# Kernel tuning notes

Hardware: AMD Instinct MI355X
Metric: run time of the kernel (lower is better)

The kernel has to match this reference:

```python
import jax, jax.numpy as jnp
import numpy as np

D_K = 64
ATTN_MASKED = True
NEG = 1.0e9


def setup_inputs() -> dict:
    key = jax.random.key(0)
    k1, k2, k3, k4 = jax.random.split(key, 4)
    B, H, S, d = 2, 16, 2048, D_K
    Q = jax.random.normal(k1, (B, H, S, d), dtype=jnp.float32)
    K = jax.random.normal(k2, (B, H, S, d), dtype=jnp.float32)
    V = jax.random.normal(k3, (B, H, S, d), dtype=jnp.float32)
    pad_mask = jax.random.randint(k4, (B, S), 0, 2, dtype=jnp.int32)
    return {"Q": Q, "K": K, "V": V, "pad_mask": pad_mask}


def reference(Q, K, V, pad_mask):
    # scores: [B, H, Sq, Sk]
    scores = jnp.einsum("bhqd,bhkd->bhqk", Q, K) / np.sqrt(D_K).astype(np.float32)
    S_out, S_in = scores.shape[-2], scores.shape[-1]
    pad = pad_mask[:, None, None, :].astype(scores.dtype)  # [B,1,1,Sk]
    if ATTN_MASKED:
        causal = jnp.triu(jnp.ones((S_out, S_in), dtype=scores.dtype), k=1)[None, None]
        mask = ((pad + causal) > 0).astype(scores.dtype)
    else:
        mask = jnp.broadcast_to(pad, scores.shape)
    scores = scores - NEG * mask
    attn = jax.nn.softmax(scores, axis=-1)
    return jnp.einsum("bhqk,bhkd->bhqd", attn, V)
```

## Files before the change

### kernel.cpp

```cpp
#include <hip/hip_runtime.h>
#include <hip/hip_bf16.h>

#define S_LEN 2048
#define DH    64
#define NBH   32
#define KVT   32
#define NT    64

typedef __attribute__((ext_vector_type(8)))  short short8;
typedef __attribute__((ext_vector_type(4)))  float f32x4;
typedef __attribute__((ext_vector_type(16))) float f32x16;

static __device__ __forceinline__ unsigned cvtpk_bf16(float a, float b) {
    unsigned r;
    asm("v_cvt_pk_bf16_f32 %0, %1, %2" : "=v"(r) : "v"(a), "v"(b));
    return r;
}
static __device__ __forceinline__ float xor32_max(float x) {
    return fmaxf(x, __shfl_xor(x, 32));
}
static __device__ __forceinline__ float xor32_add(float x) {
    return x + __shfl_xor(x, 32);
}

__global__ __launch_bounds__(256)
void prep_kernel(const float* __restrict__ K, const float* __restrict__ V,
                 char* __restrict__ Kimg, char* __restrict__ Vimg)
{
    const int t = blockIdx.x, bh = blockIdx.y, tid = threadIdx.x;
    const long tileOff = ((long)bh * NT + t) * 4096;
    const float* kp = K + (long)bh * S_LEN * DH + t * KVT * DH;
    const float* vp = V + (long)bh * S_LEN * DH + t * KVT * DH;

    {
        int key = tid >> 3, dc = tid & 7;
        f32x4 x = *(const f32x4*)(kp + key * 64 + dc * 8);
        f32x4 y = *(const f32x4*)(kp + key * 64 + dc * 8 + 4);
        uint4 w;
        w.x = cvtpk_bf16(x[0], x[1]);
        w.y = cvtpk_bf16(x[2], x[3]);
        w.z = cvtpk_bf16(y[0], y[1]);
        w.w = cvtpk_bf16(y[2], y[3]);
        *(uint4*)(Kimg + tileOff + key * 128 + dc * 16) = w;
    }
    {
        int vdg = tid & 15, vkq = tid >> 4;
        int d0 = vdg * 4, k0 = vkq * 2;
        f32x4 x0 = *(const f32x4*)(vp + k0 * 64 + d0);
        f32x4 x1 = *(const f32x4*)(vp + (k0 + 1) * 64 + d0);
        #pragma unroll
        for (int i = 0; i < 4; ++i)
            *(unsigned*)(Vimg + tileOff + (d0 + i) * 64 + k0 * 2) = cvtpk_bf16(x0[i], x1[i]);
    }
}

__global__ void fz_kernel(const int* __restrict__ pad, int* __restrict__ fz)
{
    int b = blockIdx.x;
    __shared__ int red[256];
    int local = S_LEN;
    for (int k = threadIdx.x; k < S_LEN; k += 256)
        if (pad[b * S_LEN + k] == 0 && k < local) local = k;
    red[threadIdx.x] = local;
    __syncthreads();
    for (int s = 128; s > 0; s >>= 1) {
        if (threadIdx.x < s) red[threadIdx.x] = min(red[threadIdx.x], red[threadIdx.x + s]);
        __syncthreads();
    }
    if (threadIdx.x == 0) fz[b] = red[0];
}

__global__ __launch_bounds__(1024)
void bias_kernel(const int* __restrict__ pad, float* __restrict__ bias)
{
    int b = blockIdx.x;
    #pragma unroll
    for (int i = 0; i < 2; ++i) {
        int k = threadIdx.x + i * 1024;
        bias[b * S_LEN + k] = pad[b * S_LEN + k] ? -1e30f : 0.f;
    }
}

__global__ __launch_bounds__(1024)
void meanv_kernel(const float* __restrict__ V, const int* __restrict__ fz,
                  float* __restrict__ meanv)
{
    const int bh = blockIdx.x;
    const int b  = bh >> 4;
    if (fz[b] <= 0) return;
    const int d4 = threadIdx.x & 15;
    const int kp = threadIdx.x >> 4;
    const float* vp = V + (long)bh * S_LEN * DH;
    f32x4 acc = (f32x4){0.f, 0.f, 0.f, 0.f};
    #pragma unroll 4
    for (int k = kp; k < S_LEN; k += 64)
        acc += *(const f32x4*)(vp + (long)k * DH + d4 * 4);
    __shared__ f32x4 red[64][16];
    red[kp][d4] = acc;
    __syncthreads();
    #pragma unroll
    for (int s = 32; s >= 1; s >>= 1) {
        if (kp < s) red[kp][d4] += red[kp + s][d4];
        __syncthreads();
    }
    if (kp == 0)
        *(f32x4*)(meanv + bh * DH + d4 * 4) = red[0][d4] * (1.0f / 2048.0f);
}

#define LOADK(dst, tt) do { const char* _p = KB + (long)(tt) * 4096 + lq * 128 + hi * 16; \
    dst[0] = *(const short8*)(_p);       dst[1] = *(const short8*)(_p + 32);  \
    dst[2] = *(const short8*)(_p + 64);  dst[3] = *(const short8*)(_p + 96); } while (0)
#define LOADV(dst, tt) do { const char* _p = VB + (long)(tt) * 4096 + lq * 64 + hi * 16; \
    dst[0] = *(const short8*)(_p);        dst[1] = *(const short8*)(_p + 32); \
    dst[2] = *(const short8*)(_p + 2048); dst[3] = *(const short8*)(_p + 2048 + 32); } while (0)
#define LOADB(dst, tt) do { const float* _p = biasB + (tt) * 32 + hi * 4; \
    dst[0] = *(const f32x4*)(_p);      dst[1] = *(const f32x4*)(_p + 8); \
    dst[2] = *(const f32x4*)(_p + 16); dst[3] = *(const f32x4*)(_p + 24); } while (0)

#define COMPUTE(TT, K_, V_, B_) do {                                          \
    f32x16 s0;                                                                \
    _Pragma("unroll")                                                         \
    for (int g = 0; g < 4; ++g) {                                             \
        f32x4 pb4 = B_[g];                                                    \
        _Pragma("unroll")                                                     \
        for (int i = 0; i < 4; ++i) s0[g * 4 + i] = pb4[i];                   \
    }                                                                         \
    __builtin_amdgcn_s_setprio(1);                                            \
    s0 = __builtin_amdgcn_mfma_f32_32x32x16_bf16(K_[0], bq[0], s0, 0, 0, 0);  \
    s0 = __builtin_amdgcn_mfma_f32_32x32x16_bf16(K_[1], bq[1], s0, 0, 0, 0);  \
    s0 = __builtin_amdgcn_mfma_f32_32x32x16_bf16(K_[2], bq[2], s0, 0, 0, 0);  \
    s0 = __builtin_amdgcn_mfma_f32_32x32x16_bf16(K_[3], bq[3], s0, 0, 0, 0);  \
    __builtin_amdgcn_s_setprio(0);                                            \
    if ((TT) == nkv - 1) {                                                    \
        _Pragma("unroll")                                                     \
        for (int rr = 0; rr < 16; ++rr) {                                     \
            int key_r = (rr & 3) + 8 * (rr >> 2) + 4 * hi;                    \
            if (key_r > lq) s0[rr] = -1e30f;                                  \
        }                                                                     \
    }                                                                         \
    float bm = s0[0];                                                         \
    _Pragma("unroll")                                                         \
    for (int rr = 1; rr < 16; ++rr) bm = fmaxf(bm, s0[rr]);                   \
    bm = xor32_max(bm);                                                       \
    if (__any(bm > m_run + 8.0f)) {                                           \
        float mnew = fmaxf(m_run, bm);                                        \
        float c = exp2f(m_run - mnew);                                        \
        m_run = mnew; l_run *= c;                                             \
        _Pragma("unroll")                                                     \
        for (int rr = 0; rr < 16; ++rr) { o0[rr] *= c; o1[rr] *= c; }         \
    }                                                                         \
    float rs = 0.f;                                                           \
    _Pragma("unroll")                                                         \
    for (int rr = 0; rr < 16; ++rr) {                                         \
        float p = exp2f(s0[rr] - m_run);                                      \
        s0[rr] = p; rs += p;                                                  \
    }                                                                         \
    l_run += xor32_add(rs);                                                   \
    short8 pfr0, pfr1;                                                        \
    {                                                                         \
        unsigned a0 = cvtpk_bf16(s0[0], s0[1]), b0 = cvtpk_bf16(s0[4], s0[5]);\
        asm("v_permlane32_swap_b32 %0, %1" : "+v"(a0), "+v"(b0));             \
        unsigned a1 = cvtpk_bf16(s0[2], s0[3]), b1 = cvtpk_bf16(s0[6], s0[7]);\
        asm("v_permlane32_swap_b32 %0, %1" : "+v"(a1), "+v"(b1));             \
        union { short8 s8; unsigned u[4]; } u;                                \
        u.u[0] = a0; u.u[1] = a1; u.u[2] = b0; u.u[3] = b1;                   \
        pfr0 = u.s8;                                                          \
    }                                                                         \
    {                                                                         \
        unsigned a0 = cvtpk_bf16(s0[8], s0[9]),  b0 = cvtpk_bf16(s0[12], s0[13]); \
        asm("v_permlane32_swap_b32 %0, %1" : "+v"(a0), "+v"(b0));             \
        unsigned a1 = cvtpk_bf16(s0[10], s0[11]), b1 = cvtpk_bf16(s0[14], s0[15]); \
        asm("v_permlane32_swap_b32 %0, %1" : "+v"(a1), "+v"(b1));             \
        union { short8 s8; unsigned u[4]; } u;                                \
        u.u[0] = a0; u.u[1] = a1; u.u[2] = b0; u.u[3] = b1;                   \
        pfr1 = u.s8;                                                          \
    }                                                                         \
    __builtin_amdgcn_s_setprio(1);                                            \
    o0 = __builtin_amdgcn_mfma_f32_32x32x16_bf16(V_[0], pfr0, o0, 0, 0, 0);   \
    o0 = __builtin_amdgcn_mfma_f32_32x32x16_bf16(V_[1], pfr1, o0, 0, 0, 0);   \
    o1 = __builtin_amdgcn_mfma_f32_32x32x16_bf16(V_[2], pfr0, o1, 0, 0, 0);   \
    o1 = __builtin_amdgcn_mfma_f32_32x32x16_bf16(V_[3], pfr1, o1, 0, 0, 0);   \
    __builtin_amdgcn_s_setprio(0);                                            \
} while (0)

__global__ __launch_bounds__(64, 2)
void attn_fwd7(const float* __restrict__ Q, const char* __restrict__ Kimg,
               const char* __restrict__ Vimg, const float* __restrict__ bias,
               float* __restrict__ out)
{
    const int lane = threadIdx.x;
    const int lq = lane & 31, hi = lane >> 5;

    const int gid = blockIdx.x;
    const int x   = gid & 7;
    const int c   = (gid >> 3) & 31;
    const int m   = (gid >> 8) & 3;
    const int s   = gid >> 10;
    const int bh  = x + 8 * (c & 3);
    const int e   = ((c >> 2) << 2) | m;
    const int bx  = s ? 63 - e : e;
    const int q0  = bx * 32;
    const int nkv = bx + 1;
    const long base = (long)bh * S_LEN * DH;

    const char*  KB    = Kimg + (long)bh * NT * 4096;
    const char*  VB    = Vimg + (long)bh * NT * 4096;
    const float* biasB = bias + (bh >> 4) * S_LEN;

    const float QS = 0.18033688011112042f;
    short8 bq[4];
    {
        const float* qp = Q + base + (long)(q0 + lq) * DH;
        #pragma unroll
        for (int ss = 0; ss < 4; ++ss) {
            int d0 = ss * 16 + hi * 8;
            f32x4 xx = *(const f32x4*)(qp + d0);
            f32x4 yy = *(const f32x4*)(qp + d0 + 4);
            union { short8 s8; unsigned u4[4]; } uu;
            uu.u4[0] = cvtpk_bf16(xx[0] * QS, xx[1] * QS);
            uu.u4[1] = cvtpk_bf16(xx[2] * QS, xx[3] * QS);
            uu.u4[2] = cvtpk_bf16(yy[0] * QS, yy[1] * QS);
            uu.u4[3] = cvtpk_bf16(yy[2] * QS, yy[3] * QS);
            bq[ss] = uu.s8;
        }
    }

    f32x16 o0, o1;
    #pragma unroll
    for (int rr = 0; rr < 16; ++rr) { o0[rr] = 0.f; o1[rr] = 0.f; }
    float m_run = -1e30f, l_run = 0.f;

    short8 kA[4], kB_[4], kC[4], vA[4], vB_[4], vC[4];
    f32x4  bA[4], bB_[4], bC[4];

    LOADB(bA, 0);  LOADK(kA, 0);  LOADV(vA, 0);
    if (nkv > 1) { LOADB(bB_, 1); LOADK(kB_, 1); LOADV(vB_, 1); }

    int t = 0;
    for (;;) {
        if (t + 2 < nkv) { LOADB(bC, t + 2);  LOADK(kC, t + 2);  LOADV(vC, t + 2); }
        COMPUTE(t, kA, vA, bA);
        ++t; if (t >= nkv) break;
        if (t + 2 < nkv) { LOADB(bA, t + 2);  LOADK(kA, t + 2);  LOADV(vA, t + 2); }
        COMPUTE(t, kB_, vB_, bB_);
        ++t; if (t >= nkv) break;
        if (t + 2 < nkv) { LOADB(bB_, t + 2); LOADK(kB_, t + 2); LOADV(vB_, t + 2); }
        COMPUTE(t, kC, vC, bC);
        ++t; if (t >= nkv) break;
    }

    float invl = 1.0f / l_run;
    float* op = out + base + (long)(q0 + lq) * DH;
    #pragma unroll
    for (int g = 0; g < 4; ++g) {
        f32x4 w0, w1;
        #pragma unroll
        for (int i = 0; i < 4; ++i) {
            w0[i] = o0[g * 4 + i] * invl;
            w1[i] = o1[g * 4 + i] * invl;
        }
        *(f32x4*)(op + g * 8 + hi * 4)      = w0;
        *(f32x4*)(op + 32 + g * 8 + hi * 4) = w1;
    }
}

__global__ void fixup_kernel(const int* __restrict__ fz, const float* __restrict__ meanv,
                             float* __restrict__ out)
{
    const int bh = blockIdx.x;
    const int b  = bh >> 4;
    const int n  = fz[b];
    if (n <= 0) return;
    __shared__ float mv[DH];
    if (threadIdx.x < DH) mv[threadIdx.x] = meanv[bh * DH + threadIdx.x];
    __syncthreads();
    float* op = out + (long)bh * S_LEN * DH;
    for (int i = threadIdx.x; i < n * DH; i += 256) op[i] = mv[i & 63];
}

extern "C" void kernel_launch(void* const* d_in, const int* in_sizes, int n_in,
                              void* d_out, int out_size, void* d_ws, size_t ws_size,
                              hipStream_t stream)
{
    const float* Q   = (const float*)d_in[0];
    const float* K   = (const float*)d_in[1];
    const float* V   = (const float*)d_in[2];
    const int*   pad = (const int*)d_in[3];
    float* out = (float*)d_out;

    int*   fz    = (int*)d_ws;
    float* meanv = (float*)((char*)d_ws + 256);
    float* bias  = (float*)((char*)d_ws + 8448);
    char*  Kimg  = (char*)d_ws + 32768;
    char*  Vimg  = Kimg + (size_t)NBH * NT * 4096;

    fz_kernel<<<dim3(2), dim3(256), 0, stream>>>(pad, fz);
    bias_kernel<<<dim3(2), dim3(1024), 0, stream>>>(pad, bias);
    prep_kernel<<<dim3(NT, NBH), dim3(256), 0, stream>>>(K, V, Kimg, Vimg);
    attn_fwd7<<<dim3(2048), dim3(64), 0, stream>>>(Q, Kimg, Vimg, bias, out);
    meanv_kernel<<<dim3(NBH), dim3(1024), 0, stream>>>(V, fz, meanv);
    fixup_kernel<<<dim3(NBH), dim3(256), 0, stream>>>(fz, meanv, out);
}
```

Before: 94.11 us.

## Split KV loop across four waves per block with LDS softmax merge

Each block now runs four waves that stride over the KV tiles of one 32-query tile. Their partial max, sum and output accumulators are combined through shared memory by wave 0 using a flash-decoding style rescale. This targets the long serial KV loops of late causal tiles, which limited latency and parallelism with one wave per block. It adds LDS traffic, a block barrier and idle waves on short tiles. The row max and row sum reductions are also rewritten as trees to shorten the dependency chains.

```diff
diff --git a/kernel.cpp b/kernel.cpp
--- a/kernel.cpp
+++ b/kernel.cpp
@@ -138,9 +138,11 @@
             if (key_r > lq) s0[rr] = -1e30f;                                  \
         }                                                                     \
     }                                                                         \
-    float bm = s0[0];                                                         \
+    float bmg[4];                                                             \
     _Pragma("unroll")                                                         \
-    for (int rr = 1; rr < 16; ++rr) bm = fmaxf(bm, s0[rr]);                   \
+    for (int g = 0; g < 4; ++g)                                               \
+        bmg[g] = fmaxf(fmaxf(s0[g*4], s0[g*4+1]), fmaxf(s0[g*4+2], s0[g*4+3])); \
+    float bm = fmaxf(fmaxf(bmg[0], bmg[1]), fmaxf(bmg[2], bmg[3]));           \
     bm = xor32_max(bm);                                                       \
     if (__any(bm > m_run + 8.0f)) {                                           \
         float mnew = fmaxf(m_run, bm);                                        \
@@ -149,12 +151,13 @@
         _Pragma("unroll")                                                     \
         for (int rr = 0; rr < 16; ++rr) { o0[rr] *= c; o1[rr] *= c; }         \
     }                                                                         \
-    float rs = 0.f;                                                           \
     _Pragma("unroll")                                                         \
-    for (int rr = 0; rr < 16; ++rr) {                                         \
-        float p = exp2f(s0[rr] - m_run);                                      \
-        s0[rr] = p; rs += p;                                                  \
-    }                                                                         \
+    for (int rr = 0; rr < 16; ++rr) s0[rr] = exp2f(s0[rr] - m_run);           \
+    float rsg[4];                                                             \
+    _Pragma("unroll")                                                         \
+    for (int g = 0; g < 4; ++g)                                               \
+        rsg[g] = (s0[g*4] + s0[g*4+1]) + (s0[g*4+2] + s0[g*4+3]);             \
+    float rs = (rsg[0] + rsg[1]) + (rsg[2] + rsg[3]);                         \
     l_run += xor32_add(rs);                                                   \
     short8 pfr0, pfr1;                                                        \
     {                                                                         \
@@ -183,13 +186,19 @@
     __builtin_amdgcn_s_setprio(0);                                            \
 } while (0)
 
-__global__ __launch_bounds__(64, 2)
-void attn_fwd7(const float* __restrict__ Q, const char* __restrict__ Kimg,
+__global__ __launch_bounds__(256, 3)
+void attn_fwd8(const float* __restrict__ Q, const char* __restrict__ Kimg,
                const char* __restrict__ Vimg, const float* __restrict__ bias,
                float* __restrict__ out)
 {
-    const int lane = threadIdx.x;
-    const int lq = lane & 31, hi = lane >> 5;
+    __shared__ float mW[4][32];
+    __shared__ float lW[4][32];
+    __shared__ __align__(16) char ldsO[3][8192];
+
+    const int tid  = threadIdx.x;
+    const int lane = tid & 63;
+    const int w    = tid >> 6;
+    const int lq   = lane & 31, hi = lane >> 5;
 
     const int gid = blockIdx.x;
     const int x   = gid & 7;
@@ -230,37 +239,72 @@
     for (int rr = 0; rr < 16; ++rr) { o0[rr] = 0.f; o1[rr] = 0.f; }
     float m_run = -1e30f, l_run = 0.f;
 
-    short8 kA[4], kB_[4], kC[4], vA[4], vB_[4], vC[4];
-    f32x4  bA[4], bB_[4], bC[4];
-
-    LOADB(bA, 0);  LOADK(kA, 0);  LOADV(vA, 0);
-    if (nkv > 1) { LOADB(bB_, 1); LOADK(kB_, 1); LOADV(vB_, 1); }
-
-    int t = 0;
-    for (;;) {
-        if (t + 2 < nkv) { LOADB(bC, t + 2);  LOADK(kC, t + 2);  LOADV(vC, t + 2); }
-        COMPUTE(t, kA, vA, bA);
-        ++t; if (t >= nkv) break;
-        if (t + 2 < nkv) { LOADB(bA, t + 2);  LOADK(kA, t + 2);  LOADV(vA, t + 2); }
-        COMPUTE(t, kB_, vB_, bB_);
-        ++t; if (t >= nkv) break;
-        if (t + 2 < nkv) { LOADB(bB_, t + 2); LOADK(kB_, t + 2); LOADV(vB_, t + 2); }
-        COMPUTE(t, kC, vC, bC);
-        ++t; if (t >= nkv) break;
-    }
-
-    float invl = 1.0f / l_run;
-    float* op = out + base + (long)(q0 + lq) * DH;
-    #pragma unroll
-    for (int g = 0; g < 4; ++g) {
-        f32x4 w0, w1;
+    const int nw = (w < nkv) ? ((nkv - w + 3) >> 2) : 0;
+#define TIDX(i) (w + 4 * (i))
+
+    if (nw > 0) {
+        short8 kA[4], kB_[4], kC[4], vA[4], vB_[4], vC[4];
+        f32x4  bA[4], bB_[4], bC[4];
+
+        LOADB(bA, TIDX(0));  LOADK(kA, TIDX(0));  LOADV(vA, TIDX(0));
+        if (nw > 1) { LOADB(bB_, TIDX(1)); LOADK(kB_, TIDX(1)); LOADV(vB_, TIDX(1)); }
+
+        int i = 0;
+        for (;;) {
+            if (i + 2 < nw) { LOADB(bC, TIDX(i+2));  LOADK(kC, TIDX(i+2));  LOADV(vC, TIDX(i+2)); }
+            COMPUTE(TIDX(i), kA, vA, bA);
+            ++i; if (i >= nw) break;
+            if (i + 2 < nw) { LOADB(bA, TIDX(i+2));  LOADK(kA, TIDX(i+2));  LOADV(vA, TIDX(i+2)); }
+            COMPUTE(TIDX(i), kB_, vB_, bB_);
+            ++i; if (i >= nw) break;
+            if (i + 2 < nw) { LOADB(bB_, TIDX(i+2)); LOADK(kB_, TIDX(i+2)); LOADV(vB_, TIDX(i+2)); }
+            COMPUTE(TIDX(i), kC, vC, bC);
+            ++i; if (i >= nw) break;
+        }
+    }
+
+    mW[w][lq] = m_run;
+    lW[w][lq] = l_run;
+    if (w > 0) {
+        char* dst = ldsO[w - 1] + lane * 128;
         #pragma unroll
-        for (int i = 0; i < 4; ++i) {
-            w0[i] = o0[g * 4 + i] * invl;
-            w1[i] = o1[g * 4 + i] * invl;
+        for (int g = 0; g < 4; ++g) {
+            f32x4 a0, a1;
+            #pragma unroll
+            for (int i = 0; i < 4; ++i) { a0[i] = o0[g * 4 + i]; a1[i] = o1[g * 4 + i]; }
+            *(f32x4*)(dst + ((g       ^ (lane & 7)) * 16)) = a0;
+            *(f32x4*)(dst + (((4 + g) ^ (lane & 7)) * 16)) = a1;
         }
-        *(f32x4*)(op + g * 8 + hi * 4)      = w0;
-        *(f32x4*)(op + 32 + g * 8 + hi * 4) = w1;
+    }
+    __syncthreads();
+    if (w == 0) {
+        float m0 = mW[0][lq], m1 = mW[1][lq], m2 = mW[2][lq], m3 = mW[3][lq];
+        float ms = fmaxf(fmaxf(m0, m1), fmaxf(m2, m3));
+        float w0 = exp2f(m0 - ms), w1 = exp2f(m1 - ms);
+        float w2 = exp2f(m2 - ms), w3 = exp2f(m3 - ms);
+        float ls = ((w0 * lW[0][lq] + w1 * lW[1][lq]) + (w2 * lW[2][lq] + w3 * lW[3][lq]));
+        float invl = 1.0f / ls;
+
+        const char* s1p = ldsO[0] + lane * 128;
+        const char* s2p = ldsO[1] + lane * 128;
+        const char* s3p = ldsO[2] + lane * 128;
+        float* op = out + base + (long)(q0 + lq) * DH;
+        #pragma unroll
+        for (int g = 0; g < 4; ++g) {
+            int c0 = (g       ^ (lane & 7)) * 16;
+            int c1 = ((4 + g) ^ (lane & 7)) * 16;
+            f32x4 r10 = *(const f32x4*)(s1p + c0), r11 = *(const f32x4*)(s1p + c1);
+            f32x4 r20 = *(const f32x4*)(s2p + c0), r21 = *(const f32x4*)(s2p + c1);
+            f32x4 r30 = *(const f32x4*)(s3p + c0), r31 = *(const f32x4*)(s3p + c1);
+            f32x4 a0, a1;
+            #pragma unroll
+            for (int i = 0; i < 4; ++i) {
+                a0[i] = ((o0[g*4+i] * w0 + r10[i] * w1) + (r20[i] * w2 + r30[i] * w3)) * invl;
+                a1[i] = ((o1[g*4+i] * w0 + r11[i] * w1) + (r21[i] * w2 + r31[i] * w3)) * invl;
+            }
+            *(f32x4*)(op + g * 8 + hi * 4)      = a0;
+            *(f32x4*)(op + 32 + g * 8 + hi * 4) = a1;
+        }
     }
 }
 
@@ -297,7 +341,7 @@
     fz_kernel<<<dim3(2), dim3(256), 0, stream>>>(pad, fz);
     bias_kernel<<<dim3(2), dim3(1024), 0, stream>>>(pad, bias);
     prep_kernel<<<dim3(NT, NBH), dim3(256), 0, stream>>>(K, V, Kimg, Vimg);
-    attn_fwd7<<<dim3(2048), dim3(64), 0, stream>>>(Q, Kimg, Vimg, bias, out);
+    attn_fwd8<<<dim3(2048), dim3(256), 0, stream>>>(Q, Kimg, Vimg, bias, out);
     meanv_kernel<<<dim3(NBH), dim3(1024), 0, stream>>>(V, fz, meanv);
     fixup_kernel<<<dim3(NBH), dim3(256), 0, stream>>>(fz, meanv, out);
 }
```

Measured after the change: 333.7 us. 255% more time.
